# Optimization experiments

Measured on AMD Instinct MI355X. Metric: run time of the kernel, lower is better.

Reference implementation:

```python
import jax, jax.numpy as jnp
import numpy as np

B, N, D, H = 4, 1024, 768, 12
DH = D // H
HIDDEN = 4 * D
EPS = 1e-6


def _layernorm(x, g, b):
    mu = jnp.mean(x, axis=-1, keepdims=True)
    var = jnp.mean(jnp.square(x - mu), axis=-1, keepdims=True)
    return (x - mu) * jax.lax.rsqrt(var + EPS) * g + b


def setup_inputs() -> dict:
    key = jax.random.key(0)
    ks = jax.random.split(key, 8)
    s = 0.02  # init scale for weights
    return {
        "x": jax.random.normal(ks[0], (B, N, D), jnp.float32),
        "adj_bias": jax.random.normal(ks[1], (N, N), jnp.float32) * 0.1,
        "ln1_g": jnp.ones((D,), jnp.float32),
        "ln1_b": jnp.zeros((D,), jnp.float32),
        "qkv_w": jax.random.normal(ks[2], (D, 3 * D), jnp.float32) * s,
        "qkv_b": jnp.zeros((3 * D,), jnp.float32),
        "proj_w": jax.random.normal(ks[3], (D, D), jnp.float32) * s,
        "proj_b": jnp.zeros((D,), jnp.float32),
        "ln2_g": jnp.ones((D,), jnp.float32),
        "ln2_b": jnp.zeros((D,), jnp.float32),
        "fc1_w": jax.random.normal(ks[4], (D, HIDDEN), jnp.float32) * s,
        "fc1_b": jnp.zeros((HIDDEN,), jnp.float32),
        "fc2_w": jax.random.normal(ks[5], (HIDDEN, D), jnp.float32) * s,
        "fc2_b": jnp.zeros((D,), jnp.float32),
    }


def reference(x, adj_bias, ln1_g, ln1_b, qkv_w, qkv_b, proj_w, proj_b,
              ln2_g, ln2_b, fc1_w, fc1_b, fc2_w, fc2_b):
    scale = DH ** -0.5
    # --- attention with additive adjacency bias ---
    h = _layernorm(x, ln1_g, ln1_b)
    qkv = (h @ qkv_w + qkv_b).reshape(B, N, 3, H, DH)
    q, k, v = (jnp.moveaxis(qkv, 2, 0)[i].transpose(0, 2, 1, 3) for i in range(3))  # [B,H,N,DH]
    scores = jnp.einsum('bhqd,bhkd->bhqk', q, k) * scale + adj_bias[None, None]
    w = jax.nn.softmax(scores, axis=-1)
    attn = jnp.einsum('bhqk,bhkd->bhqd', w, v)          # [B,H,N,DH]
    attn = attn.transpose(0, 2, 1, 3).reshape(B, N, D)  # [B,N,D]
    x = x + (attn @ proj_w + proj_b)
    # --- MLP ---
    h2 = _layernorm(x, ln2_g, ln2_b)
    m = jax.nn.gelu(h2 @ fc1_w + fc1_b, approximate=False) @ fc2_w + fc2_b
    return x + m
```

## Files before the change

### kernel.cpp

```cpp
#include <hip/hip_runtime.h>
#include <cstdint>
#include <cstring>

typedef unsigned short u16;
typedef __attribute__((ext_vector_type(8))) short short8;
typedef __attribute__((ext_vector_type(4))) float float4v;

#define BB 4
#define NN 1024
#define DD 768
#define HH 12
#define DHH 64
#define HID 3072
#define MM (BB*NN)

__device__ __forceinline__ u16 f2b(float f) {
  unsigned int u = __float_as_uint(f);
  u += 0x7FFF + ((u >> 16) & 1);
  return (u16)(u >> 16);
}
__device__ __forceinline__ float b2f(u16 h) {
  return __uint_as_float(((unsigned int)h) << 16);
}

__device__ __forceinline__ void gll16(const void* g, void* l) {
  __builtin_amdgcn_global_load_lds(
      (const __attribute__((address_space(1))) unsigned int*)g,
      (__attribute__((address_space(3))) unsigned int*)l, 16, 0, 0);
}

__global__ __launch_bounds__(256)
void prep_k(const float* __restrict__ qkvw, const float* __restrict__ projw,
            const float* __restrict__ fc1w, const float* __restrict__ fc2w,
            const float* __restrict__ adj,
            u16* __restrict__ wtqkv, u16* __restrict__ wtproj,
            u16* __restrict__ wtfc1, u16* __restrict__ wtfc2,
            u16* __restrict__ adjP) {
  __shared__ float tile[32][33];
  const int id = blockIdx.x, t = threadIdx.x;
  if (id < 6912) {
    const float* w; u16* wt; int K, N, tid;
    if (id < 1728)      { w = qkvw;  wt = wtqkv;  K = DD;  N = 3 * DD; tid = id; }
    else if (id < 2304) { w = projw; wt = wtproj; K = DD;  N = DD;     tid = id - 1728; }
    else if (id < 4608) { w = fc1w;  wt = wtfc1;  K = DD;  N = HID;    tid = id - 2304; }
    else                { w = fc2w;  wt = wtfc2;  K = HID; N = DD;     tid = id - 4608; }
    const int ntiles = N / 32;
    const int n0 = (tid % ntiles) * 32, k0 = (tid / ntiles) * 32;
    const int tx = t & 31, ty = t >> 5;
#pragma unroll
    for (int i = 0; i < 4; i++)
      tile[ty + i * 8][tx] = w[(size_t)(k0 + ty + i * 8) * N + n0 + tx];
    __syncthreads();
#pragma unroll
    for (int i = 0; i < 4; i++)
      wt[(size_t)(n0 + ty + i * 8) * K + k0 + tx] = f2b(tile[tx][ty + i * 8]);
  } else {
    const int aid = id - 6912;
    const int qt = aid >> 4, kt = aid & 15;
    const int wv = t >> 6, q4 = (t >> 4) & 3, m15 = t & 15;
    u16 v[16];
#pragma unroll
    for (int ct = 0; ct < 4; ct++)
#pragma unroll
      for (int r = 0; r < 4; r++)
        v[ct * 4 + r] =
            f2b(adj[(size_t)(qt * 64 + wv * 16 + q4 * 4 + r) * NN + kt * 64 + ct * 16 + m15]);
    u16* dst = adjP + (size_t)aid * 4096 + t * 16;
    *(uint4*)dst = *(const uint4*)&v[0];
    *(uint4*)(dst + 8) = *(const uint4*)&v[8];
  }
}

__global__ __launch_bounds__(256)
void ln_k(const float* __restrict__ x, const float* __restrict__ g,
          const float* __restrict__ b, u16* __restrict__ o) {
  const int row = blockIdx.x, t = threadIdx.x;
  const float* xr = x + (size_t)row * DD;
  float v0 = xr[t], v1 = xr[t + 256], v2 = xr[t + 512];
  float s = v0 + v1 + v2;
  float s2 = v0 * v0 + v1 * v1 + v2 * v2;
#pragma unroll
  for (int off = 32; off > 0; off >>= 1) {
    s += __shfl_down(s, off);
    s2 += __shfl_down(s2, off);
  }
  __shared__ float rs[4], rs2[4], bc[2];
  const int lane = t & 63, wv = t >> 6;
  if (lane == 0) { rs[wv] = s; rs2[wv] = s2; }
  __syncthreads();
  if (t == 0) {
    float ts = rs[0] + rs[1] + rs[2] + rs[3];
    float ts2 = rs2[0] + rs2[1] + rs2[2] + rs2[3];
    float mean = ts * (1.f / DD);
    float var = ts2 * (1.f / DD) - mean * mean;
    bc[0] = mean;
    bc[1] = rsqrtf(var + 1e-6f);
  }
  __syncthreads();
  const float mean = bc[0], rstd = bc[1];
  u16* orow = o + (size_t)row * DD;
  orow[t]       = f2b((v0 - mean) * rstd * g[t]       + b[t]);
  orow[t + 256] = f2b((v1 - mean) * rstd * g[t + 256] + b[t + 256]);
  orow[t + 512] = f2b((v2 - mean) * rstd * g[t + 512] + b[t + 512]);
}

template <int MODE, int TN>
__global__ __launch_bounds__(256, 4)
void gemm_k(const u16* __restrict__ A, const u16* __restrict__ Bt,
            const float* __restrict__ bias, const float* __restrict__ resid,
            float* __restrict__ outf, u16* __restrict__ outb,
            u16* __restrict__ outq, u16* __restrict__ outk, u16* __restrict__ outv,
            int M, int N, int K) {
  __shared__ u16 As[2][128 * 32];
  __shared__ u16 Bs[2][TN * 32];
  constexpr int JM = TN / 32;
  constexpr int VC = (TN == 128) ? 4 : 3;
  const int tileM = blockIdx.y * 128, tileN = blockIdx.x * TN;
  const int lane = threadIdx.x & 63, wave = threadIdx.x >> 6;
  const int wrow = (wave >> 1) * 64, wcol = (wave & 1) * (TN / 2);
  const int m15 = lane & 15, q4 = lane >> 4;

  float4v acc[4][JM];
#pragma unroll
  for (int i = 0; i < 4; i++)
#pragma unroll
    for (int j = 0; j < JM; j++) acc[i][j] = (float4v)0.f;

  auto stage = [&](int kt, int buf) {
    const int kk0 = kt * 32;
#pragma unroll
    for (int q = wave; q < 8; q += 4) {
      const int c = q * 64 + lane;
      gll16(A + (size_t)(tileM + (c >> 2)) * K + kk0 + (c & 3) * 8, &As[buf][q * 512]);
    }
#pragma unroll
    for (int q = wave; q < TN / 16; q += 4) {
      const int c = q * 64 + lane;
      gll16(Bt + (size_t)(tileN + (c >> 2)) * K + kk0 + (c & 3) * 8, &Bs[buf][q * 512]);
    }
  };

  const int T = K >> 5;
  stage(0, 0);
  for (int kt = 0; kt < T; ++kt) {
    const int cur = kt & 1;
    if (kt + 1 < T) {
      stage(kt + 1, cur ^ 1);
      asm volatile("s_waitcnt vmcnt(%0)\n\ts_barrier" :: "n"(VC) : "memory");
    } else {
      asm volatile("s_waitcnt vmcnt(0)\n\ts_barrier" ::: "memory");
    }
    short8 af[4], bfr[JM];
#pragma unroll
    for (int i = 0; i < 4; i++)
      af[i] = *(const short8*)(&As[cur][(wrow + i * 16 + m15) * 32 + q4 * 8]);
#pragma unroll
    for (int j = 0; j < JM; j++)
      bfr[j] = *(const short8*)(&Bs[cur][(wcol + j * 16 + m15) * 32 + q4 * 8]);
#pragma unroll
    for (int i = 0; i < 4; i++)
#pragma unroll
      for (int j = 0; j < JM; j++)
        acc[i][j] = __builtin_amdgcn_mfma_f32_16x16x32_bf16(af[i], bfr[j], acc[i][j], 0, 0, 0);
    asm volatile("s_waitcnt lgkmcnt(0)\n\ts_barrier" ::: "memory");
  }

#pragma unroll
  for (int i = 0; i < 4; i++) {
#pragma unroll
    for (int j = 0; j < JM; j++) {
      const int col = tileN + wcol + j * 16 + m15;
#pragma unroll
      for (int r = 0; r < 4; r++) {
        const int row = tileM + wrow + i * 16 + q4 * 4 + r;
        float v = acc[i][j][r] + bias[col];
        if (MODE == 1) {
          outf[(size_t)row * N + col] = resid[(size_t)row * N + col] + v;
        } else if (MODE == 2) {
          float gv = 0.5f * v * (1.f + erff(v * 0.70710678f));
          outb[(size_t)row * N + col] = f2b(gv);
        } else {
          const int three = col / DD, hh = (col % DD) >> 6, dh = col & 63;
          const int bb = row >> 10, nn = row & 1023;
          if (three == 2) {
            outv[(((size_t)(bb * HH + hh)) * DHH + dh) * NN + nn] = f2b(v);
          } else {
            const size_t idx = (((size_t)(bb * HH + hh)) * NN + nn) * DHH + dh;
            (three == 0 ? outq : outk)[idx] = f2b(v);
          }
        }
      }
    }
  }
}

__global__ __launch_bounds__(256, 4)
void attn_k(const u16* __restrict__ qw, const u16* __restrict__ kw,
            const u16* __restrict__ vtw, const u16* __restrict__ adjP,
            u16* __restrict__ out) {
  __shared__ u16 Ks[64][72];
  __shared__ u16 Vt[64][72];
  __shared__ u16 Pb[4][16][72];

  const int qt = blockIdx.x, bh = blockIdx.y;
  const int t = threadIdx.x, lane = t & 63, wave = t >> 6;
  const int m15 = lane & 15, q4 = lane >> 4;

  const u16* qrow = qw + ((size_t)bh * NN + qt * 64 + wave * 16 + m15) * DHH;
  const short8 qf0 = *(const short8*)(qrow + q4 * 8);
  const short8 qf1 = *(const short8*)(qrow + 32 + q4 * 8);

  float lreg[4] = {0.f, 0.f, 0.f, 0.f};
  float4v o[4];
#pragma unroll
  for (int ct = 0; ct < 4; ct++) o[ct] = (float4v)0.f;

  const u16* kbase0 = kw + (size_t)bh * NN * DHH;
  const u16* vtbase0 = vtw + (size_t)bh * DHH * NN;
  const u16* abase = adjP + (size_t)qt * 16 * 4096 + t * 16;

  const int r0 = t >> 3;
  const int c80 = (t & 7) * 8;

  uint4 kr0 = *(const uint4*)(kbase0 + r0 * 64 + c80);
  uint4 kr1 = *(const uint4*)(kbase0 + (r0 + 32) * 64 + c80);
  uint4 vr0 = *(const uint4*)(vtbase0 + (size_t)r0 * NN + c80);
  uint4 vr1 = *(const uint4*)(vtbase0 + (size_t)(r0 + 32) * NN + c80);

  for (int kt = 0; kt < 16; kt++) {
    __syncthreads();
    *(uint4*)&Ks[r0][c80] = kr0;
    *(uint4*)&Ks[r0 + 32][c80] = kr1;
    *(uint4*)&Vt[r0][c80] = vr0;
    *(uint4*)&Vt[r0 + 32][c80] = vr1;
    __syncthreads();
    if (kt < 15) {
      const u16* kb = kbase0 + (size_t)(kt + 1) * 64 * DHH;
      const u16* vb = vtbase0 + (kt + 1) * 64;
      kr0 = *(const uint4*)(kb + r0 * 64 + c80);
      kr1 = *(const uint4*)(kb + (r0 + 32) * 64 + c80);
      vr0 = *(const uint4*)(vb + (size_t)r0 * NN + c80);
      vr1 = *(const uint4*)(vb + (size_t)(r0 + 32) * NN + c80);
    }
    u16 av[16];
    const u16* ap = abase + (size_t)kt * 4096;
    *(uint4*)&av[0] = *(const uint4*)ap;
    *(uint4*)&av[8] = *(const uint4*)(ap + 8);

    float4v s[4];
#pragma unroll
    for (int ct = 0; ct < 4; ct++) s[ct] = (float4v)0.f;
#pragma unroll
    for (int ct = 0; ct < 4; ct++) {
      short8 b = *(const short8*)&Ks[ct * 16 + m15][q4 * 8];
      s[ct] = __builtin_amdgcn_mfma_f32_16x16x32_bf16(qf0, b, s[ct], 0, 0, 0);
    }
#pragma unroll
    for (int ct = 0; ct < 4; ct++) {
      short8 b = *(const short8*)&Ks[ct * 16 + m15][32 + q4 * 8];
      s[ct] = __builtin_amdgcn_mfma_f32_16x16x32_bf16(qf1, b, s[ct], 0, 0, 0);
    }

#pragma unroll
    for (int ct = 0; ct < 4; ct++)
#pragma unroll
      for (int r = 0; r < 4; r++) {
        float v = s[ct][r] * 0.125f + b2f(av[ct * 4 + r]);
        u16 pb = f2b(__expf(v));
        Pb[wave][q4 * 4 + r][ct * 16 + m15] = pb;
        lreg[r] += b2f(pb);
      }

    asm volatile("s_waitcnt lgkmcnt(0)" ::: "memory");

    short8 a0 = *(const short8*)&Pb[wave][m15][q4 * 8];
    short8 a1 = *(const short8*)&Pb[wave][m15][32 + q4 * 8];
#pragma unroll
    for (int ct = 0; ct < 4; ct++) {
      short8 b = *(const short8*)&Vt[ct * 16 + m15][q4 * 8];
      o[ct] = __builtin_amdgcn_mfma_f32_16x16x32_bf16(a0, b, o[ct], 0, 0, 0);
    }
#pragma unroll
    for (int ct = 0; ct < 4; ct++) {
      short8 b = *(const short8*)&Vt[ct * 16 + m15][32 + q4 * 8];
      o[ct] = __builtin_amdgcn_mfma_f32_16x16x32_bf16(a1, b, o[ct], 0, 0, 0);
    }
  }

#pragma unroll
  for (int off = 1; off < 16; off <<= 1)
#pragma unroll
    for (int r = 0; r < 4; r++) lreg[r] += __shfl_xor(lreg[r], off);

  const int bb2 = bh / HH, hh = bh % HH;
  const int row0 = qt * 64 + wave * 16 + q4 * 4;
#pragma unroll
  for (int ct = 0; ct < 4; ct++)
#pragma unroll
    for (int r = 0; r < 4; r++)
      out[((size_t)(bb2 * NN + row0 + r)) * DD + hh * 64 + ct * 16 + m15] =
          f2b(o[ct][r] / lreg[r]);
}

extern "C" void kernel_launch(void* const* d_in, const int* in_sizes, int n_in,
                              void* d_out, int out_size, void* d_ws, size_t ws_size,
                              hipStream_t stream) {
  const float* x     = (const float*)d_in[0];
  const float* adj   = (const float*)d_in[1];
  const float* ln1g  = (const float*)d_in[2];
  const float* ln1b  = (const float*)d_in[3];
  const float* qkvw  = (const float*)d_in[4];
  const float* qkvb  = (const float*)d_in[5];
  const float* projw = (const float*)d_in[6];
  const float* projb = (const float*)d_in[7];
  const float* ln2g  = (const float*)d_in[8];
  const float* ln2b  = (const float*)d_in[9];
  const float* fc1w  = (const float*)d_in[10];
  const float* fc1b  = (const float*)d_in[11];
  const float* fc2w  = (const float*)d_in[12];
  const float* fc2b  = (const float*)d_in[13];
  float* out = (float*)d_out;

  char* ws = (char*)d_ws;
  u16* wtqkv = (u16*)ws;  ws += (size_t)DD * (3 * DD) * 2;
  u16* wtproj = (u16*)ws; ws += (size_t)DD * DD * 2;
  u16* wtfc1 = (u16*)ws;  ws += (size_t)DD * HID * 2;
  u16* wtfc2 = (u16*)ws;  ws += (size_t)HID * DD * 2;
  u16* adjP = (u16*)ws;   ws += (size_t)NN * NN * 2;
  u16* hbuf = (u16*)ws;   ws += (size_t)MM * DD * 2;
  u16* qws = (u16*)ws;    ws += (size_t)MM * DD * 2;
  u16* kws = (u16*)ws;    ws += (size_t)MM * DD * 2;
  u16* vtws = (u16*)ws;   ws += (size_t)MM * DD * 2;
  u16* attnb = (u16*)ws;  ws += (size_t)MM * DD * 2;
  u16* h2buf = (u16*)ws;  ws += (size_t)MM * DD * 2;
  u16* a1buf = (u16*)ws;  ws += (size_t)MM * HID * 2;

  prep_k<<<7168, 256, 0, stream>>>(qkvw, projw, fc1w, fc2w, adj,
                                   wtqkv, wtproj, wtfc1, wtfc2, adjP);

  ln_k<<<MM, 256, 0, stream>>>(x, ln1g, ln1b, hbuf);

  gemm_k<0, 128><<<dim3((3 * DD) / 128, MM / 128), 256, 0, stream>>>(
      hbuf, wtqkv, qkvb, nullptr, nullptr, nullptr, qws, kws, vtws, MM, 3 * DD, DD);

  attn_k<<<dim3(NN / 64, BB * HH), 256, 0, stream>>>(qws, kws, vtws, adjP, attnb);

  gemm_k<1, 64><<<dim3(DD / 64, MM / 128), 256, 0, stream>>>(
      attnb, wtproj, projb, x, out, nullptr, nullptr, nullptr, nullptr, MM, DD, DD);

  ln_k<<<MM, 256, 0, stream>>>(out, ln2g, ln2b, h2buf);

  gemm_k<2, 128><<<dim3(HID / 128, MM / 128), 256, 0, stream>>>(
      h2buf, wtfc1, fc1b, nullptr, nullptr, a1buf, nullptr, nullptr, nullptr, MM, HID, DD);

  gemm_k<1, 64><<<dim3(DD / 64, MM / 128), 256, 0, stream>>>(
      a1buf, wtfc2, fc2b, out, out, nullptr, nullptr, nullptr, nullptr, MM, DD, HID);
}
```

Measured before the change: 289.8 us.

## Deepen GEMM prefetch pipeline, swizzle LDS tiles, remap blocks to XCDs

```diff
diff --git a/kernel.cpp b/kernel.cpp
--- a/kernel.cpp
+++ b/kernel.cpp
@@ -104,21 +104,30 @@
   orow[t + 512] = f2b((v2 - mean) * rstd * g[t + 512] + b[t + 512]);
 }
 
-template <int MODE, int TN>
+template <int MODE, int TN, int NC>
 __global__ __launch_bounds__(256, 4)
 void gemm_k(const u16* __restrict__ A, const u16* __restrict__ Bt,
             const float* __restrict__ bias, const float* __restrict__ resid,
             float* __restrict__ outf, u16* __restrict__ outb,
             u16* __restrict__ outq, u16* __restrict__ outk, u16* __restrict__ outv,
-            int M, int N, int K) {
-  __shared__ u16 As[2][128 * 32];
-  __shared__ u16 Bs[2][TN * 32];
+            int K) {
+  constexpr int DP = (TN == 64) ? 4 : 3;
+  __shared__ u16 As[DP][128 * 32];
+  __shared__ u16 Bs[DP][TN * 32];
   constexpr int JM = TN / 32;
   constexpr int VC = (TN == 128) ? 4 : 3;
-  const int tileM = blockIdx.y * 128, tileN = blockIdx.x * TN;
+  constexpr int NB = NC / TN;
+  constexpr int RN = NB / 2;
+
+  const int id = blockIdx.x;
+  const int xcd = id & 7, idx = id >> 3;
+  const int tileN = ((xcd & 1) * RN + idx % RN) * TN;
+  const int tileM = ((xcd >> 1) * 8 + idx / RN) * 128;
+
   const int lane = threadIdx.x & 63, wave = threadIdx.x >> 6;
   const int wrow = (wave >> 1) * 64, wcol = (wave & 1) * (TN / 2);
   const int m15 = lane & 15, q4 = lane >> 4;
+  const int sw = (q4 ^ ((m15 >> 1) & 3)) * 8;
 
   float4v acc[4][JM];
 #pragma unroll
@@ -131,39 +140,60 @@
 #pragma unroll
     for (int q = wave; q < 8; q += 4) {
       const int c = q * 64 + lane;
-      gll16(A + (size_t)(tileM + (c >> 2)) * K + kk0 + (c & 3) * 8, &As[buf][q * 512]);
+      gll16(A + (size_t)(tileM + (c >> 2)) * K + kk0 + ((c & 3) ^ ((c >> 3) & 3)) * 8,
+            &As[buf][q * 512]);
     }
 #pragma unroll
     for (int q = wave; q < TN / 16; q += 4) {
       const int c = q * 64 + lane;
-      gll16(Bt + (size_t)(tileN + (c >> 2)) * K + kk0 + (c & 3) * 8, &Bs[buf][q * 512]);
+      gll16(Bt + (size_t)(tileN + (c >> 2)) * K + kk0 + ((c & 3) ^ ((c >> 3) & 3)) * 8,
+            &Bs[buf][q * 512]);
     }
   };
 
-  const int T = K >> 5;
-  stage(0, 0);
-  for (int kt = 0; kt < T; ++kt) {
-    const int cur = kt & 1;
-    if (kt + 1 < T) {
-      stage(kt + 1, cur ^ 1);
-      asm volatile("s_waitcnt vmcnt(%0)\n\ts_barrier" :: "n"(VC) : "memory");
-    } else {
-      asm volatile("s_waitcnt vmcnt(0)\n\ts_barrier" ::: "memory");
-    }
+  auto compute = [&](int buf) {
     short8 af[4], bfr[JM];
 #pragma unroll
     for (int i = 0; i < 4; i++)
-      af[i] = *(const short8*)(&As[cur][(wrow + i * 16 + m15) * 32 + q4 * 8]);
+      af[i] = *(const short8*)(&As[buf][(wrow + i * 16 + m15) * 32 + sw]);
 #pragma unroll
     for (int j = 0; j < JM; j++)
-      bfr[j] = *(const short8*)(&Bs[cur][(wcol + j * 16 + m15) * 32 + q4 * 8]);
+      bfr[j] = *(const short8*)(&Bs[buf][(wcol + j * 16 + m15) * 32 + sw]);
 #pragma unroll
     for (int i = 0; i < 4; i++)
 #pragma unroll
       for (int j = 0; j < JM; j++)
         acc[i][j] = __builtin_amdgcn_mfma_f32_16x16x32_bf16(af[i], bfr[j], acc[i][j], 0, 0, 0);
+  };
+
+  const int T = K >> 5;
+#pragma unroll
+  for (int d = 0; d < DP; d++) stage(d, d);
+
+  int cur = 0;
+  for (int kt = 0; kt < T - DP; ++kt) {
+    asm volatile("s_waitcnt vmcnt(%0)\n\ts_barrier" :: "n"((DP - 1) * VC) : "memory");
+    compute(cur);
     asm volatile("s_waitcnt lgkmcnt(0)\n\ts_barrier" ::: "memory");
-  }
+    stage(kt + DP, cur);
+    cur = (cur == DP - 1) ? 0 : cur + 1;
+  }
+  if constexpr (DP == 4) {
+    asm volatile("s_waitcnt vmcnt(%0)\n\ts_barrier" :: "n"(3 * VC) : "memory");
+    compute(cur);
+    asm volatile("s_waitcnt lgkmcnt(0)\n\ts_barrier" ::: "memory");
+    cur = (cur == DP - 1) ? 0 : cur + 1;
+  }
+  asm volatile("s_waitcnt vmcnt(%0)\n\ts_barrier" :: "n"(2 * VC) : "memory");
+  compute(cur);
+  asm volatile("s_waitcnt lgkmcnt(0)\n\ts_barrier" ::: "memory");
+  cur = (cur == DP - 1) ? 0 : cur + 1;
+  asm volatile("s_waitcnt vmcnt(%0)\n\ts_barrier" :: "n"(VC) : "memory");
+  compute(cur);
+  asm volatile("s_waitcnt lgkmcnt(0)\n\ts_barrier" ::: "memory");
+  cur = (cur == DP - 1) ? 0 : cur + 1;
+  asm volatile("s_waitcnt vmcnt(0)\n\ts_barrier" ::: "memory");
+  compute(cur);
 
 #pragma unroll
   for (int i = 0; i < 4; i++) {
@@ -175,18 +205,18 @@
         const int row = tileM + wrow + i * 16 + q4 * 4 + r;
         float v = acc[i][j][r] + bias[col];
         if (MODE == 1) {
-          outf[(size_t)row * N + col] = resid[(size_t)row * N + col] + v;
+          outf[(size_t)row * NC + col] = resid[(size_t)row * NC + col] + v;
         } else if (MODE == 2) {
           float gv = 0.5f * v * (1.f + erff(v * 0.70710678f));
-          outb[(size_t)row * N + col] = f2b(gv);
+          outb[(size_t)row * NC + col] = f2b(gv);
         } else {
           const int three = col / DD, hh = (col % DD) >> 6, dh = col & 63;
           const int bb = row >> 10, nn = row & 1023;
           if (three == 2) {
             outv[(((size_t)(bb * HH + hh)) * DHH + dh) * NN + nn] = f2b(v);
           } else {
-            const size_t idx = (((size_t)(bb * HH + hh)) * NN + nn) * DHH + dh;
-            (three == 0 ? outq : outk)[idx] = f2b(v);
+            const size_t idx2 = (((size_t)(bb * HH + hh)) * NN + nn) * DHH + dh;
+            (three == 0 ? outq : outk)[idx2] = f2b(v);
           }
         }
       }
@@ -202,7 +232,9 @@
   __shared__ u16 Vt[64][72];
   __shared__ u16 Pb[4][16][72];
 
-  const int qt = blockIdx.x, bh = blockIdx.y;
+  const int id = blockIdx.x;
+  const int bh = (id & 7) * 6 + ((id >> 3) >> 4);
+  const int qt = (id >> 3) & 15;
   const int t = threadIdx.x, lane = t & 63, wave = t >> 6;
   const int m15 = lane & 15, q4 = lane >> 4;
 
@@ -340,19 +372,19 @@
 
   ln_k<<<MM, 256, 0, stream>>>(x, ln1g, ln1b, hbuf);
 
-  gemm_k<0, 128><<<dim3((3 * DD) / 128, MM / 128), 256, 0, stream>>>(
-      hbuf, wtqkv, qkvb, nullptr, nullptr, nullptr, qws, kws, vtws, MM, 3 * DD, DD);
-
-  attn_k<<<dim3(NN / 64, BB * HH), 256, 0, stream>>>(qws, kws, vtws, adjP, attnb);
-
-  gemm_k<1, 64><<<dim3(DD / 64, MM / 128), 256, 0, stream>>>(
-      attnb, wtproj, projb, x, out, nullptr, nullptr, nullptr, nullptr, MM, DD, DD);
+  gemm_k<0, 128, 3 * DD><<<((3 * DD) / 128) * (MM / 128), 256, 0, stream>>>(
+      hbuf, wtqkv, qkvb, nullptr, nullptr, nullptr, qws, kws, vtws, DD);
+
+  attn_k<<<(NN / 64) * (BB * HH), 256, 0, stream>>>(qws, kws, vtws, adjP, attnb);
+
+  gemm_k<1, 64, DD><<<(DD / 64) * (MM / 128), 256, 0, stream>>>(
+      attnb, wtproj, projb, x, out, nullptr, nullptr, nullptr, nullptr, DD);
 
   ln_k<<<MM, 256, 0, stream>>>(out, ln2g, ln2b, h2buf);
 
-  gemm_k<2, 128><<<dim3(HID / 128, MM / 128), 256, 0, stream>>>(
-      h2buf, wtfc1, fc1b, nullptr, nullptr, a1buf, nullptr, nullptr, nullptr, MM, HID, DD);
-
-  gemm_k<1, 64><<<dim3(DD / 64, MM / 128), 256, 0, stream>>>(
-      a1buf, wtfc2, fc2b, out, out, nullptr, nullptr, nullptr, nullptr, MM, DD, HID);
-}
+  gemm_k<2, 128, HID><<<(HID / 128) * (MM / 128), 256, 0, stream>>>(
+      h2buf, wtfc1, fc1b, nullptr, nullptr, a1buf, nullptr, nullptr, nullptr, DD);
+
+  gemm_k<1, 64, DD><<<(DD / 64) * (MM / 128), 256, 0, stream>>>(
+      a1buf, wtfc2, fc2b, out, out, nullptr, nullptr, nullptr, nullptr, HID);
+}
```

New measurement: 305.3 us. +5.4%, slower.
